# Optimization experiments

Hardware: AMD Instinct MI355X
Metric: run time of the kernel (lower is better)

The kernel has to match this reference:

```python
import jax, jax.numpy as jnp
import numpy as np

B, T, IN = 8, 1000, 80
CONV = 256
CCEP = 222            # ltv_out_channels
FFT_SIZE = 1024
HOP = 256
WIN = 2 * HOP         # 512
PAD = (FFT_SIZE - CCEP) // 2   # 401
NFFT = 2048


def _conv1d_same(x, W, b, groups):
    # x: (B,T,C); W: (O, C//groups, 3); equivalent to torch Conv1d pad=2 then [1:-1]
    y = jax.lax.conv_general_dilated(
        jnp.transpose(x, (0, 2, 1)), W, (1,), [(1, 1)],
        feature_group_count=groups,
        dimension_numbers=('NCH', 'OIH', 'NCH'))
    return jnp.transpose(y, (0, 2, 1)) + b


def _forward(x, z, W1, b1, W2, b2, W3, b3, W4, b4):
    Bx, Tx, _ = x.shape
    # ---- ConvLayers ----
    h = jax.nn.relu(_conv1d_same(x, W1, b1, 1))
    h = jax.nn.relu(_conv1d_same(h, W2, b2, 8))
    h = jax.nn.relu(_conv1d_same(h, W3, b3, 8))
    ccep = _conv1d_same(h, W4, b4, 1)            # (B,T,222)
    q = jnp.arange(1, CCEP // 2 + 1, dtype=x.dtype)
    quef = jnp.concatenate([q[::-1], q])          # [111..1,1..111]
    ccep = ccep / quef
    # ---- ccep -> impulse (log-magnitude cepstrum -> minimum-ish phase impulse) ----
    c = jnp.pad(ccep, ((0, 0), (0, 0), (PAD, PAD)))           # (B,T,1024)
    Y = jnp.fft.fft(c, n=FFT_SIZE, axis=-1)
    mag = jnp.power(10.0, Y.real)
    imp = jnp.fft.ifft(mag * jnp.exp(1j * Y.imag), n=FFT_SIZE, axis=-1).real  # (B,T,1024)
    # ---- time-varying impulse convolution (cross-correlation per frame) ----
    L = z.shape[-1]
    zz = z.reshape(Bx, 1, L)
    zp = jnp.pad(zz, ((0, 0), (0, 0), (WIN // 2 - 1, WIN // 2)))
    starts = jnp.arange(Tx) * HOP
    frames = zp[:, :, starts[:, None] + jnp.arange(WIN)]       # (B,1,T,512)
    fp = jnp.pad(frames, ((0, 0), (0, 0), (0, 0), (FFT_SIZE // 2 - 1, FFT_SIZE // 2)))  # len 1535
    # corr[s] = sum_k fp[s+k] * imp[k], s in [0,512); linear corr via zero-padded FFT
    Fz = jnp.fft.rfft(fp, n=NFFT, axis=-1)                     # (B,1,T,NFFT//2+1)
    Fy = jnp.fft.rfft(imp, n=NFFT, axis=-1)[:, None]           # (B,1,T,NFFT//2+1)
    corr = jnp.fft.irfft(Fz * jnp.conj(Fy), n=NFFT, axis=-1)[..., :WIN]  # (B,1,T,512)
    # ---- overlap-add ----
    n = jnp.arange(WIN, dtype=x.dtype)
    win = 0.5 * (1.0 - jnp.cos(2.0 * jnp.pi * n / WIN))        # periodic hann, win_norm=1
    zw = corr * win
    l, r = zw[..., :HOP], zw[..., HOP:]
    out = l + jnp.roll(r, 1, axis=2)
    return out.reshape(Bx, 1, Tx * HOP)


def setup_inputs() -> dict:
    key = jax.random.key(0)
    ks = jax.random.split(key, 12)
    x = jax.random.normal(ks[0], (B, T, IN), dtype=jnp.float32)
    z = jax.random.normal(ks[1], (B, 1, T * HOP), dtype=jnp.float32)
    def w(k, o, i, kk, scale):
        return jax.random.normal(k, (o, i, kk), dtype=jnp.float32) * (scale / np.sqrt(i * kk))
    W1 = w(ks[2], CONV, IN, 3, 1.0)
    b1 = jnp.zeros((CONV,), jnp.float32)
    W2 = w(ks[3], CONV, CONV // 8, 3, 1.0)
    b2 = jnp.zeros((CONV,), jnp.float32)
    W3 = w(ks[4], CONV, CONV // 8, 3, 1.0)
    b3 = jnp.zeros((CONV,), jnp.float32)
    W4 = w(ks[5], CCEP, CONV, 3, 0.01)   # small scale keeps 10**(.) well-conditioned
    b4 = jnp.zeros((CCEP,), jnp.float32)
    return {"x": x, "z": z, "W1": W1, "b1": b1, "W2": W2, "b2": b2,
            "W3": W3, "b3": b3, "W4": W4, "b4": b4}


def reference(x, z, W1, b1, W2, b2, W3, b3, W4, b4):
    return _forward(x, z, W1, b1, W2, b2, W3, b3, W4, b4)
```

## Files before the change

kernel.cpp:

```cpp
#include <hip/hip_runtime.h>
#include <hip/hip_bf16.h>

#define T_LEN 1000
#define B_N 8
#define IN_CH 80
#define CONV_CH 256
#define CCEP_N 222

typedef short s8v __attribute__((ext_vector_type(8)));
typedef float f16v __attribute__((ext_vector_type(16)));

#define TWO_PI 6.28318530717958647692f

__global__ __launch_bounds__(256) void k_prep(
    const float* __restrict__ W1, const float* __restrict__ W2,
    const float* __restrict__ W3, const float* __restrict__ W4,
    float* __restrict__ Wt1, float* __restrict__ Wt2, float* __restrict__ Wt3,
    __hip_bfloat16* __restrict__ Wc, float2* __restrict__ twTab,
    float* __restrict__ winTab) {
  const int bid = blockIdx.x, tid = threadIdx.x;
  if (bid < 240) {
    int e = bid * 256 + tid;
    int o = e / 240, k = e - o * 240;
    Wt1[k * 256 + o] = W1[e];
  } else if (bid < 336) {
    int e = (bid - 240) * 256 + tid;
    int o = e / 96, k = e - o * 96;
    Wt2[k * 256 + o] = W2[e];
  } else if (bid < 432) {
    int e = (bid - 336) * 256 + tid;
    int o = e / 96, k = e - o * 96;
    Wt3[k * 256 + o] = W3[e];
  } else if (bid < 1200) {
    int e = (bid - 432) * 256 + tid;
    int kloc = e & 31, n = (e >> 5) & 255, chg = e >> 13;
    int kp = chg * 32 + kloc;
    int kappa = kp >> 8, i = kp & 255;
    float v = 0.f;
    if (n < CCEP_N) {
      float invq = 1.f / (float)((n < 111) ? (111 - n) : (n - 110));
      v = W4[n * 768 + i * 3 + kappa] * invq;
    }
    Wc[e] = __float2bfloat16(v);
  } else {
    int e = (bid - 1200) * 256 + tid;
    if (e < 1020) {
      int Q, off;
      if (e < 768)       { Q = 256; off = 0; }
      else if (e < 960)  { Q = 64;  off = 768; }
      else if (e < 1008) { Q = 16;  off = 960; }
      else               { Q = 4;   off = 1008; }
      int rem = e - off;
      int r = rem / Q, pos = rem - r * Q;
      float ang = (TWO_PI * (float)((r + 1) * pos)) / (float)(4 * Q);
      float s, c;
      sincosf(ang, &s, &c);
      twTab[e] = make_float2(c, s);
    } else if (e < 1532) {
      int n = e - 1020;
      winTab[n] = (0.5f - 0.5f * cosf(TWO_PI * (float)n / 512.f)) * (1.f / 1024.f);
    }
  }
}

__global__ __launch_bounds__(256) void k_convall(const float* __restrict__ x,
    const float* __restrict__ Wt1, const float* __restrict__ b1,
    const float* __restrict__ Wt2, const float* __restrict__ b2,
    const float* __restrict__ Wt3, const float* __restrict__ b3,
    __hip_bfloat16* __restrict__ out) {
  const int b = blockIdx.y;
  const int t0 = blockIdx.x * 10;
  const int o = threadIdx.x;
  const int cb = (o >> 5) << 5;
  __shared__ float xs[IN_CH * 18];
  __shared__ float hs1[CONV_CH * 14];
  __shared__ float hs2[CONV_CH * 14];
  for (int e = threadIdx.x; e < 16 * IN_CH; e += 256) {
    int r = e / IN_CH, c = e - r * IN_CH;
    int t = t0 - 3 + r;
    xs[c * 18 + r] = (t >= 0 && t < T_LEN) ? x[(b * T_LEN + t) * IN_CH + c] : 0.f;
  }
  __syncthreads();
  {
    float acc[14];
    float bv = b1[o];
#pragma unroll
    for (int j = 0; j < 14; j++) acc[j] = bv;
    for (int i = 0; i < IN_CH; i++) {
      float w0 = Wt1[(3 * i + 0) * 256 + o];
      float w1 = Wt1[(3 * i + 1) * 256 + o];
      float w2 = Wt1[(3 * i + 2) * 256 + o];
      const float* row = &xs[i * 18];
      float a[16];
#pragma unroll
      for (int u = 0; u < 8; u++) *(float2*)&a[2 * u] = *(const float2*)(row + 2 * u);
#pragma unroll
      for (int j = 0; j < 14; j++) {
        acc[j] = fmaf(a[j], w0, acc[j]);
        acc[j] = fmaf(a[j + 1], w1, acc[j]);
        acc[j] = fmaf(a[j + 2], w2, acc[j]);
      }
    }
#pragma unroll
    for (int j = 0; j < 14; j++) {
      int t = t0 - 2 + j;
      hs1[o * 14 + j] = (t >= 0 && t < T_LEN) ? fmaxf(acc[j], 0.f) : 0.f;
    }
  }
  __syncthreads();
  {
    float acc[12];
    float bv = b2[o];
#pragma unroll
    for (int j = 0; j < 12; j++) acc[j] = bv;
    for (int i = 0; i < 32; i++) {
      float w0 = Wt2[(3 * i + 0) * 256 + o];
      float w1 = Wt2[(3 * i + 1) * 256 + o];
      float w2 = Wt2[(3 * i + 2) * 256 + o];
      const float* row = &hs1[(cb + i) * 14];
      float a[14];
#pragma unroll
      for (int u = 0; u < 7; u++) *(float2*)&a[2 * u] = *(const float2*)(row + 2 * u);
#pragma unroll
      for (int j = 0; j < 12; j++) {
        acc[j] = fmaf(a[j], w0, acc[j]);
        acc[j] = fmaf(a[j + 1], w1, acc[j]);
        acc[j] = fmaf(a[j + 2], w2, acc[j]);
      }
    }
    __syncthreads();
#pragma unroll
    for (int j = 0; j < 12; j++) {
      int t = t0 - 1 + j;
      hs2[o * 14 + j] = (t >= 0 && t < T_LEN) ? fmaxf(acc[j], 0.f) : 0.f;
    }
  }
  __syncthreads();
  {
    float acc[10];
    float bv = b3[o];
#pragma unroll
    for (int j = 0; j < 10; j++) acc[j] = bv;
    for (int i = 0; i < 32; i++) {
      float w0 = Wt3[(3 * i + 0) * 256 + o];
      float w1 = Wt3[(3 * i + 1) * 256 + o];
      float w2 = Wt3[(3 * i + 2) * 256 + o];
      const float* row = &hs2[(cb + i) * 14];
      float a[12];
#pragma unroll
      for (int u = 0; u < 6; u++) *(float2*)&a[2 * u] = *(const float2*)(row + 2 * u);
#pragma unroll
      for (int j = 0; j < 10; j++) {
        acc[j] = fmaf(a[j], w0, acc[j]);
        acc[j] = fmaf(a[j + 1], w1, acc[j]);
        acc[j] = fmaf(a[j + 2], w2, acc[j]);
      }
    }
#pragma unroll
    for (int j = 0; j < 10; j++)
      out[(b * T_LEN + t0 + j) * CONV_CH + o] = __float2bfloat16(fmaxf(acc[j], 0.f));
  }
}

#define APITCH 264
#define BPITCH 40
#define PSTRIDE 1792000
__global__ __launch_bounds__(256) void k_conv4m(
    const __hip_bfloat16* __restrict__ h3, const __hip_bfloat16* __restrict__ Wc,
    const float* __restrict__ bias, float* __restrict__ Pbase) {
  const int mb = blockIdx.x, b = blockIdx.y, ks = blockIdx.z;
  float* __restrict__ P = Pbase + (size_t)ks * PSTRIDE;
  const int t0 = mb * 64;
  const int tid = threadIdx.x;
  const int w = tid >> 6, lane = tid & 63;
  const int wm = w >> 1, wn = w & 1;
  const int lm = lane & 31, half = lane >> 5;

  __shared__ short h3s[67 * APITCH];
  __shared__ short Bs[2][256 * BPITCH];

  const ushort* h3u = (const ushort*)h3;
  for (int g = tid; g < 67 * 64; g += 256) {
    int rr = g >> 6, c4 = g & 63;
    int t = t0 + rr - 1;
    uint2 v = make_uint2(0u, 0u);
    if (t >= 0 && t < T_LEN)
      v = *(const uint2*)(h3u + (b * T_LEN + t) * CONV_CH + c4 * 4);
    *(uint2*)(h3s + rr * APITCH + c4 * 4) = v;
  }

  const ushort* Wu = (const ushort*)(Wc) + (size_t)(ks * 6) * 8192;
#pragma unroll
  for (int it = 0; it < 4; ++it) {
    int idx = (it * 256 + tid) * 8;
    uint4 v = *(const uint4*)(Wu + idx);
    int n = idx >> 5, kloc = idx & 31;
    *(uint4*)(Bs[0] + n * BPITCH + kloc) = v;
  }
  __syncthreads();

  f16v acc0 = {}, acc1 = {}, acc2 = {}, acc3 = {};

  for (int ch = 0; ch < 6; ++ch) {
    const int p = ch & 1;
    if (ch < 5) {
      const ushort* src = Wu + (ch + 1) * 8192;
#pragma unroll
      for (int it = 0; it < 4; ++it) {
        int idx = (it * 256 + tid) * 8;
        uint4 v = *(const uint4*)(src + idx);
        int n = idx >> 5, kloc = idx & 31;
        *(uint4*)(Bs[p ^ 1] + n * BPITCH + kloc) = v;
      }
    }
#pragma unroll
    for (int s = 0; s < 2; ++s) {
      int k0 = ks * 192 + ch * 32 + s * 16;
      int kappa = k0 >> 8, i0 = k0 & 255;
      s8v a = *(const s8v*)(h3s + (wm * 32 + lm + kappa) * APITCH + i0 + half * 8);
      const short* bp = Bs[p] + (wn * 128 + lm) * BPITCH + s * 16 + half * 8;
      s8v b0 = *(const s8v*)(bp);
      s8v b1 = *(const s8v*)(bp + 32 * BPITCH);
      s8v b2 = *(const s8v*)(bp + 64 * BPITCH);
      s8v b3 = *(const s8v*)(bp + 96 * BPITCH);
      acc0 = __builtin_amdgcn_mfma_f32_32x32x16_bf16(a, b0, acc0, 0, 0, 0);
      acc1 = __builtin_amdgcn_mfma_f32_32x32x16_bf16(a, b1, acc1, 0, 0, 0);
      acc2 = __builtin_amdgcn_mfma_f32_32x32x16_bf16(a, b2, acc2, 0, 0, 0);
      acc3 = __builtin_amdgcn_mfma_f32_32x32x16_bf16(a, b3, acc3, 0, 0, 0);
    }
    __syncthreads();
  }

  const int col = lm;
#pragma unroll
  for (int nt = 0; nt < 4; ++nt) {
    int c = wn * 128 + nt * 32 + col;
    if (c >= CCEP_N) continue;
    float bq = 0.f;
    if (ks == 0) {
      float invq = 1.f / (float)((c < 111) ? (111 - c) : (c - 110));
      bq = bias[c] * invq;
    }
    const f16v* A = (nt == 0) ? &acc0 : (nt == 1) ? &acc1 : (nt == 2) ? &acc2 : &acc3;
#pragma unroll
    for (int reg = 0; reg < 16; ++reg) {
      int row = (reg & 3) + 8 * (reg >> 2) + 4 * half;
      int t = t0 + wm * 32 + row;
      if (t < T_LEN)
        P[(size_t)(b * T_LEN + t) * 224 + c] = (*A)[reg] + bq;
    }
  }
}

__device__ __forceinline__ float2 cmul(float2 a, float2 b) {
  return make_float2(fmaf(a.x, b.x, -(a.y * b.y)), fmaf(a.x, b.y, a.y * b.x));
}
__device__ __forceinline__ float2 cadd(float2 a, float2 b) { return make_float2(a.x + b.x, a.y + b.y); }
__device__ __forceinline__ float2 csub(float2 a, float2 b) { return make_float2(a.x - b.x, a.y - b.y); }

#define LIDX(i) ((i) + ((i) >> 2))

template <int Q, int OFF>
__device__ __forceinline__ void fwd_stage2(float2* __restrict__ A,
    float2* __restrict__ B, const float2* __restrict__ Tw, int j) {
  const int pos = j & (Q - 1);
  const int base = ((j - pos) << 2) + pos;
  float2 e1 = Tw[OFF + pos], e2 = Tw[OFF + Q + pos], e3 = Tw[OFF + 2 * Q + pos];
  const float2 w1 = make_float2(e1.x, -e1.y);
  const float2 w2 = make_float2(e2.x, -e2.y);
  const float2 w3 = make_float2(e3.x, -e3.y);
#pragma unroll
  for (int arr = 0; arr < 2; ++arr) {
    float2* X = arr ? B : A;
    float2 a = X[LIDX(base)], b = X[LIDX(base + Q)];
    float2 cc = X[LIDX(base + 2 * Q)], d = X[LIDX(base + 3 * Q)];
    float2 t0 = cadd(a, cc), t1 = csub(a, cc), t2 = cadd(b, d), bd = csub(b, d);
    float2 t3 = make_float2(bd.y, -bd.x);
    X[LIDX(base)]         = cadd(t0, t2);
    X[LIDX(base + Q)]     = cmul(cadd(t1, t3), w1);
    X[LIDX(base + 2 * Q)] = cmul(csub(t0, t2), w2);
    X[LIDX(base + 3 * Q)] = cmul(csub(t1, t3), w3);
  }
}

template <int Q, int OFF>
__device__ __forceinline__ void inv_stage_t(float2* __restrict__ X,
    const float2* __restrict__ Tw, int j) {
  const int pos = j & (Q - 1);
  const int base = ((j - pos) << 2) + pos;
  const float2 w1 = Tw[OFF + pos];
  const float2 w2 = Tw[OFF + Q + pos];
  const float2 w3 = Tw[OFF + 2 * Q + pos];
  float2 a = X[LIDX(base)];
  float2 b = cmul(X[LIDX(base + Q)], w1);
  float2 cc = cmul(X[LIDX(base + 2 * Q)], w2);
  float2 d = cmul(X[LIDX(base + 3 * Q)], w3);
  float2 t0 = cadd(a, cc), t1 = csub(a, cc), t2 = cadd(b, d), bd = csub(b, d);
  float2 t3 = make_float2(-bd.y, bd.x);
  X[LIDX(base)]         = cadd(t0, t2);
  X[LIDX(base + Q)]     = cadd(t1, t3);
  X[LIDX(base + 2 * Q)] = csub(t0, t2);
  X[LIDX(base + 3 * Q)] = csub(t1, t3);
}

__device__ __forceinline__ int rev4d(int v) {
  return ((v & 3) << 6) | (((v >> 2) & 3) << 4) | (((v >> 4) & 3) << 2) | ((v >> 6) & 3);
}

__global__ __launch_bounds__(256) void k_fft(const float* __restrict__ Pb,
    const float* __restrict__ z, const float2* __restrict__ twg,
    const float* __restrict__ wing, float* __restrict__ out,
    float* __restrict__ sbl, float* __restrict__ sbr) {
  const int u = blockIdx.x, b = blockIdx.y;
  const int tA = 2 * u, tB = tA + 1;
  const int btA = b * T_LEN + tA, btB = btA + 1;
  const int j = threadIdx.x;
  __shared__ float2 WlA[1280];
  __shared__ float2 WlB[1280];
  __shared__ float2 Tws[1020];
  for (int e = j; e < 1020; e += 256) Tws[e] = twg[e];

  const float* zb = z + b * 256000;
  float f0A = 0.f, fS, f1B = 0.f;
  {
    int zi0 = tA * 256 + j - 255;
    f0A = (zi0 >= 0) ? zb[zi0] : 0.f;
    fS = zb[tA * 256 + j + 1];
    int zi2 = tB * 256 + j + 1;
    f1B = (zi2 < 256000) ? zb[zi2] : 0.f;
  }
  float c1A = 0.f, c2A = 0.f, c1B = 0.f, c2B = 0.f;
  if (j >= 145) {
    int mA = btA * 224 + (j - 145), mB = btB * 224 + (j - 145);
    c1A = (Pb[mA] + Pb[mA + PSTRIDE]) + (Pb[mA + 2 * PSTRIDE] + Pb[mA + 3 * PSTRIDE]);
    c1B = (Pb[mB] + Pb[mB + PSTRIDE]) + (Pb[mB + 2 * PSTRIDE] + Pb[mB + 3 * PSTRIDE]);
  }
  if (j < 111) {
    int mA = btA * 224 + (j + 111), mB = btB * 224 + (j + 111);
    c2A = (Pb[mA] + Pb[mA + PSTRIDE]) + (Pb[mA + 2 * PSTRIDE] + Pb[mA + 3 * PSTRIDE]);
    c2B = (Pb[mB] + Pb[mB + PSTRIDE]) + (Pb[mB + 2 * PSTRIDE] + Pb[mB + 3 * PSTRIDE]);
  }
  __syncthreads();

  {
    float2 e1 = Tws[j], e2 = Tws[256 + j], e3 = Tws[512 + j];
    const float2 w1 = make_float2(e1.x, -e1.y);
    const float2 w2 = make_float2(e2.x, -e2.y);
    const float2 w3 = make_float2(e3.x, -e3.y);
    {
      float2 t0 = make_float2(c2A, f0A);
      float2 t1 = make_float2(-c2A, f0A);
      float2 t2 = make_float2(c1A, fS);
      float2 t3 = make_float2(fS, -c1A);
      WlA[LIDX(j)]       = cadd(t0, t2);
      WlA[LIDX(j + 256)] = cmul(cadd(t1, t3), w1);
      WlA[LIDX(j + 512)] = cmul(csub(t0, t2), w2);
      WlA[LIDX(j + 768)] = cmul(csub(t1, t3), w3);
    }
    {
      float2 t0 = make_float2(c2B, fS);
      float2 t1 = make_float2(-c2B, fS);
      float2 t2 = make_float2(c1B, f1B);
      float2 t3 = make_float2(f1B, -c1B);
      WlB[LIDX(j)]       = cadd(t0, t2);
      WlB[LIDX(j + 256)] = cmul(cadd(t1, t3), w1);
      WlB[LIDX(j + 512)] = cmul(csub(t0, t2), w2);
      WlB[LIDX(j + 768)] = cmul(csub(t1, t3), w3);
    }
  }
  __syncthreads();

  fwd_stage2<64, 768>(WlA, WlB, Tws, j);  __syncthreads();
  fwd_stage2<16, 960>(WlA, WlB, Tws, j);  __syncthreads();
  fwd_stage2<4, 1008>(WlA, WlB, Tws, j);  __syncthreads();

  const int base = 4 * j;
  float2 XA[4], XB[4];
  {
    float2 u0 = WlA[LIDX(base)], u1 = WlA[LIDX(base + 1)];
    float2 u2 = WlA[LIDX(base + 2)], u3 = WlA[LIDX(base + 3)];
    float2 t0 = cadd(u0, u2), t1 = csub(u0, u2), t2 = cadd(u1, u3), bd = csub(u1, u3);
    float2 t3 = make_float2(bd.y, -bd.x);
    XA[0] = cadd(t0, t2); XA[1] = cadd(t1, t3); XA[2] = csub(t0, t2); XA[3] = csub(t1, t3);
  }
  {
    float2 u0 = WlB[LIDX(base)], u1 = WlB[LIDX(base + 1)];
    float2 u2 = WlB[LIDX(base + 2)], u3 = WlB[LIDX(base + 3)];
    float2 t0 = cadd(u0, u2), t1 = csub(u0, u2), t2 = cadd(u1, u3), bd = csub(u1, u3);
    float2 t3 = make_float2(bd.y, -bd.x);
    XB[0] = cadd(t0, t2); XB[1] = cadd(t1, t3); XB[2] = csub(t0, t2); XB[3] = csub(t1, t3);
  }
#pragma unroll
  for (int q = 0; q < 4; ++q) { WlA[LIDX(base + q)] = XA[q]; WlB[LIDX(base + q)] = XB[q]; }
  __syncthreads();

  const int r0 = rev4d(j);
  const bool self0 = (r0 == 0);
  const int jp = self0 ? 0 : rev4d((256 - r0) & 255);
  float2 PA[4], PB[4];
#pragma unroll
  for (int q = 0; q < 4; ++q) { PA[q] = WlA[LIDX(4 * jp + q)]; PB[q] = WlB[LIDX(4 * jp + q)]; }
  float2 Z[4];
#pragma unroll
  for (int q = 0; q < 4; ++q) {
    float2 SA, SB;
    {
      float2 A = XA[q];
      float2 Bc = self0 ? PA[(4 - q) & 3] : PA[3 - q];
      float2 Y = make_float2(0.5f * (A.x + Bc.x), 0.5f * (A.y - Bc.y));
      float2 F = make_float2(0.5f * (A.y + Bc.y), -0.5f * (A.x - Bc.x));
      float mag = __expf(Y.x * 2.30258509299404568402f);
      float sy, cy;
      __sincosf(Y.y, &sy, &cy);
      float gr = mag * cy, gi = mag * sy;
      SA = make_float2(fmaf(F.x, gr, F.y * gi), fmaf(F.x, gi, -(F.y * gr)));
    }
    {
      float2 A = XB[q];
      float2 Bc = self0 ? PB[(4 - q) & 3] : PB[3 - q];
      float2 Y = make_float2(0.5f * (A.x + Bc.x), 0.5f * (A.y - Bc.y));
      float2 F = make_float2(0.5f * (A.y + Bc.y), -0.5f * (A.x - Bc.x));
      float mag = __expf(Y.x * 2.30258509299404568402f);
      float sy, cy;
      __sincosf(Y.y, &sy, &cy);
      float gr = mag * cy, gi = mag * sy;
      SB = make_float2(fmaf(F.x, gr, F.y * gi), fmaf(F.x, gi, -(F.y * gr)));
    }
    Z[q] = make_float2(SA.x - SB.y, SA.y + SB.x);
  }
  __syncthreads();

  {
    float2 t0 = cadd(Z[0], Z[2]), t1 = csub(Z[0], Z[2]), t2 = cadd(Z[1], Z[3]), bd = csub(Z[1], Z[3]);
    float2 t3 = make_float2(-bd.y, bd.x);
    WlA[LIDX(base)]     = cadd(t0, t2);
    WlA[LIDX(base + 1)] = cadd(t1, t3);
    WlA[LIDX(base + 2)] = csub(t0, t2);
    WlA[LIDX(base + 3)] = csub(t1, t3);
  }
  __syncthreads();

  inv_stage_t<4, 1008>(WlA, Tws, j);  __syncthreads();
  inv_stage_t<16, 960>(WlA, Tws, j);  __syncthreads();
  inv_stage_t<64, 768>(WlA, Tws, j);  __syncthreads();

  {
    float2 w1 = Tws[j], w2 = Tws[256 + j], w3 = Tws[512 + j];
    float2 a = WlA[LIDX(j)];
    float2 bb = cmul(WlA[LIDX(j + 256)], w1);
    float2 cc = cmul(WlA[LIDX(j + 512)], w2);
    float2 d = cmul(WlA[LIDX(j + 768)], w3);
    float2 t0 = cadd(a, cc), t1 = csub(a, cc), t2 = cadd(bb, d), bd = csub(bb, d);
    float2 t3 = make_float2(-bd.y, bd.x);
    float2 Cj    = cadd(t0, t2);
    float2 Cj256 = cadd(t1, t3);
    int n1 = 511 - j, n2 = 255 - j;
    float wn1 = wing[n1], wn2 = wing[n2];
    float vA_l = Cj256.x * wn2;
    float vAB  = Cj.x * wn1 + Cj256.y * wn2;
    float vB_r = Cj.y * wn1;
    out[(b * T_LEN + tB) * 256 + n2] = vAB;
    int su = (b * 500 + u) * 256 + n2;
    sbl[su] = vA_l;
    sbr[su] = vB_r;
  }
}

__global__ __launch_bounds__(256) void k_even(const float* __restrict__ sbl,
    const float* __restrict__ sbr, float* __restrict__ out) {
  int idx = blockIdx.x * 256 + threadIdx.x;
  int n = idx & 255;
  int bu = idx >> 8;
  int u = bu % 500, b = bu / 500;
  int up = (u == 0) ? 499 : u - 1;
  out[(b * T_LEN + 2 * u) * 256 + n] = sbl[idx] + sbr[(b * 500 + up) * 256 + n];
}

extern "C" void kernel_launch(void* const* d_in, const int* in_sizes, int n_in,
                              void* d_out, int out_size, void* d_ws, size_t ws_size,
                              hipStream_t stream) {
  const float* x  = (const float*)d_in[0];
  const float* z  = (const float*)d_in[1];
  const float* W1 = (const float*)d_in[2];
  const float* b1 = (const float*)d_in[3];
  const float* W2 = (const float*)d_in[4];
  const float* b2 = (const float*)d_in[5];
  const float* W3 = (const float*)d_in[6];
  const float* b3 = (const float*)d_in[7];
  const float* W4 = (const float*)d_in[8];
  const float* b4 = (const float*)d_in[9];

  float* ws   = (float*)d_ws;
  __hip_bfloat16* h3bf = (__hip_bfloat16*)ws;
  float* Pb   = ws + 1024000;
  float* sbl  = ws + 8192000;
  float* sbr  = ws + 9216000;
  float* Wt1  = ws + 10240000;
  float* Wt2  = ws + 10301440;
  float* Wt3  = ws + 10326016;
  __hip_bfloat16* Wc = (__hip_bfloat16*)(ws + 10350592);
  float2* twTab = (float2*)(ws + 10448896);
  float* winTab = ws + 10450944;
  float* out = (float*)d_out;

  dim3 blk(256);
  k_prep<<<1206, blk, 0, stream>>>(W1, W2, W3, W4, Wt1, Wt2, Wt3, Wc,
                                   twTab, winTab);

  dim3 cgrid10(T_LEN / 10, B_N);
  k_convall<<<cgrid10, blk, 0, stream>>>(x, Wt1, b1, Wt2, b2, Wt3, b3, h3bf);
  dim3 g4(16, B_N, 4);
  k_conv4m<<<g4, blk, 0, stream>>>(h3bf, Wc, b4, Pb);
  dim3 gf(T_LEN / 2, B_N);
  k_fft<<<gf, blk, 0, stream>>>(Pb, z, twTab, winTab, out, sbl, sbr);
  k_even<<<4000, blk, 0, stream>>>(sbl, sbr, out);
}
```

Before: 176.8 us.

## Split conv stack time rows across two thread halves with vectorized weight loads

```diff
diff --git a/kernel.cpp b/kernel.cpp
--- a/kernel.cpp
+++ b/kernel.cpp
@@ -21,16 +21,22 @@
   const int bid = blockIdx.x, tid = threadIdx.x;
   if (bid < 240) {
     int e = bid * 256 + tid;
-    int o = e / 240, k = e - o * 240;
-    Wt1[k * 256 + o] = W1[e];
+    int i = e % 80;
+    int r = e / 80;
+    int o = r & 255, kap = r >> 8;
+    Wt1[e] = W1[o * 240 + i * 3 + kap];
   } else if (bid < 336) {
     int e = (bid - 240) * 256 + tid;
-    int o = e / 96, k = e - o * 96;
-    Wt2[k * 256 + o] = W2[e];
+    int i = e & 31;
+    int r = e >> 5;
+    int o = r & 255, kap = r >> 8;
+    Wt2[e] = W2[o * 96 + i * 3 + kap];
   } else if (bid < 432) {
     int e = (bid - 336) * 256 + tid;
-    int o = e / 96, k = e - o * 96;
-    Wt3[k * 256 + o] = W3[e];
+    int i = e & 31;
+    int r = e >> 5;
+    int o = r & 255, kap = r >> 8;
+    Wt3[e] = W3[o * 96 + i * 3 + kap];
   } else if (bid < 1200) {
     int e = (bid - 432) * 256 + tid;
     int kloc = e & 31, n = (e >> 5) & 255, chg = e >> 13;
@@ -63,102 +69,108 @@
   }
 }
 
-__global__ __launch_bounds__(256) void k_convall(const float* __restrict__ x,
+template <int SH, int NJ, int NI4, int PITCH, int NA2>
+__device__ __forceinline__ void conv_acc(const float* __restrict__ abase,
+    const float* __restrict__ w0p, const float* __restrict__ w1p,
+    const float* __restrict__ w2p, float* __restrict__ acc) {
+#pragma unroll 2
+  for (int ig = 0; ig < NI4; ++ig) {
+    float4 w0 = *(const float4*)(w0p + 4 * ig);
+    float4 w1 = *(const float4*)(w1p + 4 * ig);
+    float4 w2 = *(const float4*)(w2p + 4 * ig);
+#pragma unroll
+    for (int s = 0; s < 4; ++s) {
+      const float* row = abase + (4 * ig + s) * PITCH;
+      float a[2 * NA2];
+#pragma unroll
+      for (int u = 0; u < NA2; ++u)
+        *(float2*)&a[2 * u] = *(const float2*)(row + 2 * u);
+      const float f0 = ((const float*)&w0)[s];
+      const float f1 = ((const float*)&w1)[s];
+      const float f2 = ((const float*)&w2)[s];
+#pragma unroll
+      for (int jl = 0; jl < NJ; ++jl) {
+        acc[jl] = fmaf(a[jl + SH], f0, acc[jl]);
+        acc[jl] = fmaf(a[jl + SH + 1], f1, acc[jl]);
+        acc[jl] = fmaf(a[jl + SH + 2], f2, acc[jl]);
+      }
+    }
+  }
+}
+
+__global__ __launch_bounds__(512, 6) void k_convall(const float* __restrict__ x,
     const float* __restrict__ Wt1, const float* __restrict__ b1,
     const float* __restrict__ Wt2, const float* __restrict__ b2,
     const float* __restrict__ Wt3, const float* __restrict__ b3,
     __hip_bfloat16* __restrict__ out) {
   const int b = blockIdx.y;
   const int t0 = blockIdx.x * 10;
-  const int o = threadIdx.x;
+  const int tid = threadIdx.x;
+  const int o = tid & 255;
+  const int th = tid >> 8;
   const int cb = (o >> 5) << 5;
   __shared__ float xs[IN_CH * 18];
   __shared__ float hs1[CONV_CH * 14];
   __shared__ float hs2[CONV_CH * 14];
-  for (int e = threadIdx.x; e < 16 * IN_CH; e += 256) {
+  for (int e = tid; e < 16 * IN_CH; e += 512) {
     int r = e / IN_CH, c = e - r * IN_CH;
     int t = t0 - 3 + r;
     xs[c * 18 + r] = (t >= 0 && t < T_LEN) ? x[(b * T_LEN + t) * IN_CH + c] : 0.f;
   }
   __syncthreads();
   {
-    float acc[14];
-    float bv = b1[o];
-#pragma unroll
-    for (int j = 0; j < 14; j++) acc[j] = bv;
-    for (int i = 0; i < IN_CH; i++) {
-      float w0 = Wt1[(3 * i + 0) * 256 + o];
-      float w1 = Wt1[(3 * i + 1) * 256 + o];
-      float w2 = Wt1[(3 * i + 2) * 256 + o];
-      const float* row = &xs[i * 18];
-      float a[16];
-#pragma unroll
-      for (int u = 0; u < 8; u++) *(float2*)&a[2 * u] = *(const float2*)(row + 2 * u);
-#pragma unroll
-      for (int j = 0; j < 14; j++) {
-        acc[j] = fmaf(a[j], w0, acc[j]);
-        acc[j] = fmaf(a[j + 1], w1, acc[j]);
-        acc[j] = fmaf(a[j + 2], w2, acc[j]);
-      }
-    }
-#pragma unroll
-    for (int j = 0; j < 14; j++) {
-      int t = t0 - 2 + j;
-      hs1[o * 14 + j] = (t >= 0 && t < T_LEN) ? fmaxf(acc[j], 0.f) : 0.f;
-    }
-  }
-  __syncthreads();
-  {
-    float acc[12];
-    float bv = b2[o];
-#pragma unroll
-    for (int j = 0; j < 12; j++) acc[j] = bv;
-    for (int i = 0; i < 32; i++) {
-      float w0 = Wt2[(3 * i + 0) * 256 + o];
-      float w1 = Wt2[(3 * i + 1) * 256 + o];
-      float w2 = Wt2[(3 * i + 2) * 256 + o];
-      const float* row = &hs1[(cb + i) * 14];
-      float a[14];
-#pragma unroll
-      for (int u = 0; u < 7; u++) *(float2*)&a[2 * u] = *(const float2*)(row + 2 * u);
-#pragma unroll
-      for (int j = 0; j < 12; j++) {
-        acc[j] = fmaf(a[j], w0, acc[j]);
-        acc[j] = fmaf(a[j + 1], w1, acc[j]);
-        acc[j] = fmaf(a[j + 2], w2, acc[j]);
-      }
-    }
-    __syncthreads();
-#pragma unroll
-    for (int j = 0; j < 12; j++) {
+    float acc[7];
+    const float bv = b1[o];
+#pragma unroll
+    for (int jl = 0; jl < 7; ++jl) acc[jl] = bv;
+    const float* w0p = Wt1 + o * 80;
+    const float* w1p = Wt1 + (256 + o) * 80;
+    const float* w2p = Wt1 + (512 + o) * 80;
+    if (th == 0)
+      conv_acc<0, 7, 20, 18, 5>(&xs[0], w0p, w1p, w2p, acc);
+    else
+      conv_acc<1, 7, 20, 18, 5>(&xs[6], w0p, w1p, w2p, acc);
+#pragma unroll
+    for (int jl = 0; jl < 7; ++jl) {
+      int rr = th * 7 + jl;
+      int t = t0 - 2 + rr;
+      hs1[o * 14 + rr] = (t >= 0 && t < T_LEN) ? fmaxf(acc[jl], 0.f) : 0.f;
+    }
+  }
+  __syncthreads();
+  {
+    float acc[6];
+    const float bv = b2[o];
+#pragma unroll
+    for (int jl = 0; jl < 6; ++jl) acc[jl] = bv;
+    const float* w0p = Wt2 + o * 32;
+    const float* w1p = Wt2 + (256 + o) * 32;
+    const float* w2p = Wt2 + (512 + o) * 32;
+    conv_acc<0, 6, 8, 14, 4>(&hs1[cb * 14 + th * 6], w0p, w1p, w2p, acc);
+#pragma unroll
+    for (int jl = 0; jl < 6; ++jl) {
+      int j = th * 6 + jl;
       int t = t0 - 1 + j;
-      hs2[o * 14 + j] = (t >= 0 && t < T_LEN) ? fmaxf(acc[j], 0.f) : 0.f;
-    }
-  }
-  __syncthreads();
-  {
-    float acc[10];
-    float bv = b3[o];
-#pragma unroll
-    for (int j = 0; j < 10; j++) acc[j] = bv;
-    for (int i = 0; i < 32; i++) {
-      float w0 = Wt3[(3 * i + 0) * 256 + o];
-      float w1 = Wt3[(3 * i + 1) * 256 + o];
-      float w2 = Wt3[(3 * i + 2) * 256 + o];
-      const float* row = &hs2[(cb + i) * 14];
-      float a[12];
-#pragma unroll
-      for (int u = 0; u < 6; u++) *(float2*)&a[2 * u] = *(const float2*)(row + 2 * u);
-#pragma unroll
-      for (int j = 0; j < 10; j++) {
-        acc[j] = fmaf(a[j], w0, acc[j]);
-        acc[j] = fmaf(a[j + 1], w1, acc[j]);
-        acc[j] = fmaf(a[j + 2], w2, acc[j]);
-      }
-    }
-#pragma unroll
-    for (int j = 0; j < 10; j++)
-      out[(b * T_LEN + t0 + j) * CONV_CH + o] = __float2bfloat16(fmaxf(acc[j], 0.f));
+      hs2[o * 14 + j] = (t >= 0 && t < T_LEN) ? fmaxf(acc[jl], 0.f) : 0.f;
+    }
+  }
+  __syncthreads();
+  {
+    float acc[5];
+    const float bv = b3[o];
+#pragma unroll
+    for (int jl = 0; jl < 5; ++jl) acc[jl] = bv;
+    const float* w0p = Wt3 + o * 32;
+    const float* w1p = Wt3 + (256 + o) * 32;
+    const float* w2p = Wt3 + (512 + o) * 32;
+    if (th == 0)
+      conv_acc<0, 5, 8, 14, 4>(&hs2[cb * 14], w0p, w1p, w2p, acc);
+    else
+      conv_acc<1, 5, 8, 14, 4>(&hs2[cb * 14 + 4], w0p, w1p, w2p, acc);
+#pragma unroll
+    for (int jl = 0; jl < 5; ++jl)
+      out[(b * T_LEN + t0 + th * 5 + jl) * CONV_CH + o] =
+          __float2bfloat16(fmaxf(acc[jl], 0.f));
   }
 }
 
@@ -508,7 +520,8 @@
                                    twTab, winTab);
 
   dim3 cgrid10(T_LEN / 10, B_N);
-  k_convall<<<cgrid10, blk, 0, stream>>>(x, Wt1, b1, Wt2, b2, Wt3, b3, h3bf);
+  dim3 cblk(512);
+  k_convall<<<cgrid10, cblk, 0, stream>>>(x, Wt1, b1, Wt2, b2, Wt3, b3, h3bf);
   dim3 g4(16, B_N, 4);
   k_conv4m<<<g4, blk, 0, stream>>>(h3bf, Wc, b4, Pb);
   dim3 gf(T_LEN / 2, B_N);
```

Result: slower. 288.7 us (+63.3%).

## Retile conv stack over 60-step time tiles and 64-channel slices

Applied to the files above, without the earlier changes.

```diff
diff --git a/kernel.cpp b/kernel.cpp
--- a/kernel.cpp
+++ b/kernel.cpp
@@ -21,16 +21,16 @@
   const int bid = blockIdx.x, tid = threadIdx.x;
   if (bid < 240) {
     int e = bid * 256 + tid;
-    int o = e / 240, k = e - o * 240;
-    Wt1[k * 256 + o] = W1[e];
+    int o = e & 255, s = e >> 8;
+    Wt1[e] = W1[o * 240 + s];
   } else if (bid < 336) {
     int e = (bid - 240) * 256 + tid;
-    int o = e / 96, k = e - o * 96;
-    Wt2[k * 256 + o] = W2[e];
+    int o = e & 255, s = e >> 8;
+    Wt2[e] = W2[o * 96 + s];
   } else if (bid < 432) {
     int e = (bid - 336) * 256 + tid;
-    int o = e / 96, k = e - o * 96;
-    Wt3[k * 256 + o] = W3[e];
+    int o = e & 255, s = e >> 8;
+    Wt3[e] = W3[o * 96 + s];
   } else if (bid < 1200) {
     int e = (bid - 432) * 256 + tid;
     int kloc = e & 31, n = (e >> 5) & 255, chg = e >> 13;
@@ -63,102 +63,110 @@
   }
 }
 
+#define TTILE 60
+#define XP 66
+#define HP 66
+
+template <int NI, int PITCH>
+__device__ __forceinline__ void conv8(const float* __restrict__ act,
+    const float* __restrict__ wb, int l, float* __restrict__ acc) {
+  float cw[24], nw[24];
+#pragma unroll
+  for (int q = 0; q < 24; ++q) cw[q] = wb[(q >> 3) * 256 + (q & 7)];
+  for (int i = 0; i < NI; ++i) {
+    const float* wn = wb + min(i + 1, NI - 1) * 768;
+#pragma unroll
+    for (int q = 0; q < 24; ++q) nw[q] = wn[(q >> 3) * 256 + (q & 7)];
+    float a0 = act[i * PITCH + l];
+    float a1 = act[i * PITCH + l + 1];
+    float a2 = act[i * PITCH + l + 2];
+#pragma unroll
+    for (int oc = 0; oc < 8; ++oc)
+      acc[oc] = fmaf(a0, cw[oc], fmaf(a1, cw[8 + oc], fmaf(a2, cw[16 + oc], acc[oc])));
+#pragma unroll
+    for (int q = 0; q < 24; ++q) cw[q] = nw[q];
+  }
+}
+
 __global__ __launch_bounds__(256) void k_convall(const float* __restrict__ x,
     const float* __restrict__ Wt1, const float* __restrict__ b1,
     const float* __restrict__ Wt2, const float* __restrict__ b2,
     const float* __restrict__ Wt3, const float* __restrict__ b3,
     __hip_bfloat16* __restrict__ out) {
-  const int b = blockIdx.y;
-  const int t0 = blockIdx.x * 10;
-  const int o = threadIdx.x;
-  const int cb = (o >> 5) << 5;
-  __shared__ float xs[IN_CH * 18];
-  __shared__ float hs1[CONV_CH * 14];
-  __shared__ float hs2[CONV_CH * 14];
-  for (int e = threadIdx.x; e < 16 * IN_CH; e += 256) {
-    int r = e / IN_CH, c = e - r * IN_CH;
-    int t = t0 - 3 + r;
-    xs[c * 18 + r] = (t >= 0 && t < T_LEN) ? x[(b * T_LEN + t) * IN_CH + c] : 0.f;
-  }
-  __syncthreads();
-  {
-    float acc[14];
-    float bv = b1[o];
-#pragma unroll
-    for (int j = 0; j < 14; j++) acc[j] = bv;
-    for (int i = 0; i < IN_CH; i++) {
-      float w0 = Wt1[(3 * i + 0) * 256 + o];
-      float w1 = Wt1[(3 * i + 1) * 256 + o];
-      float w2 = Wt1[(3 * i + 2) * 256 + o];
-      const float* row = &xs[i * 18];
-      float a[16];
-#pragma unroll
-      for (int u = 0; u < 8; u++) *(float2*)&a[2 * u] = *(const float2*)(row + 2 * u);
-#pragma unroll
-      for (int j = 0; j < 14; j++) {
-        acc[j] = fmaf(a[j], w0, acc[j]);
-        acc[j] = fmaf(a[j + 1], w1, acc[j]);
-        acc[j] = fmaf(a[j + 2], w2, acc[j]);
+  const int t0 = blockIdx.x * TTILE;
+  const int b  = blockIdx.y;
+  const int O0 = blockIdx.z * 64;
+  const int tid = threadIdx.x;
+  const int l = tid & 63;
+  const int w = tid >> 6;
+  const int wrel = w * 16;
+  const int wo = __builtin_amdgcn_readfirstlane(O0 + wrel);
+  const int ri0 = (w >> 1) * 32;
+
+  __shared__ float xs[IN_CH * XP];
+  __shared__ float h1s[64 * HP];
+  __shared__ float h2s[64 * HP];
+
+  for (int e = tid; e < IN_CH * XP; e += 256) {
+    int tt = e / IN_CH, c = e - tt * IN_CH;
+    int t = t0 - 3 + tt;
+    xs[c * XP + tt] = (t >= 0 && t < T_LEN) ? x[(b * T_LEN + t) * IN_CH + c] : 0.f;
+  }
+  __syncthreads();
+
+  {
+    float acc[16];
+#pragma unroll
+    for (int h = 0; h < 2; ++h) {
+#pragma unroll
+      for (int oc = 0; oc < 8; ++oc) acc[8 * h + oc] = b1[wo + 8 * h + oc];
+      conv8<IN_CH, XP>(xs, Wt1 + wo + 8 * h, l, acc + 8 * h);
+    }
+    int t = t0 - 2 + l;
+    bool v = (t >= 0 && t < T_LEN);
+#pragma unroll
+    for (int oc = 0; oc < 16; ++oc)
+      h1s[(wrel + oc) * HP + l] = v ? fmaxf(acc[oc], 0.f) : 0.f;
+  }
+  __syncthreads();
+
+  {
+    float acc[16];
+#pragma unroll
+    for (int h = 0; h < 2; ++h) {
+#pragma unroll
+      for (int oc = 0; oc < 8; ++oc) acc[8 * h + oc] = b2[wo + 8 * h + oc];
+      conv8<32, HP>(h1s + ri0 * HP, Wt2 + wo + 8 * h, l, acc + 8 * h);
+    }
+    int t = t0 - 1 + l;
+    bool v = (t >= 0 && t < T_LEN);
+#pragma unroll
+    for (int oc = 0; oc < 16; ++oc)
+      h2s[(wrel + oc) * HP + l] = v ? fmaxf(acc[oc], 0.f) : 0.f;
+  }
+  __syncthreads();
+
+  {
+    float acc[16];
+#pragma unroll
+    for (int h = 0; h < 2; ++h) {
+#pragma unroll
+      for (int oc = 0; oc < 8; ++oc) acc[8 * h + oc] = b3[wo + 8 * h + oc];
+      conv8<32, HP>(h2s + ri0 * HP, Wt3 + wo + 8 * h, l, acc + 8 * h);
+    }
+    int t = t0 + l;
+    if (l < TTILE && t < T_LEN) {
+      uint pk[8];
+#pragma unroll
+      for (int q = 0; q < 8; ++q) {
+        __hip_bfloat16 lo = __float2bfloat16(fmaxf(acc[2 * q], 0.f));
+        __hip_bfloat16 hi = __float2bfloat16(fmaxf(acc[2 * q + 1], 0.f));
+        pk[q] = (uint)(*(ushort*)&lo) | ((uint)(*(ushort*)&hi) << 16);
       }
-    }
-#pragma unroll
-    for (int j = 0; j < 14; j++) {
-      int t = t0 - 2 + j;
-      hs1[o * 14 + j] = (t >= 0 && t < T_LEN) ? fmaxf(acc[j], 0.f) : 0.f;
-    }
-  }
-  __syncthreads();
-  {
-    float acc[12];
-    float bv = b2[o];
-#pragma unroll
-    for (int j = 0; j < 12; j++) acc[j] = bv;
-    for (int i = 0; i < 32; i++) {
-      float w0 = Wt2[(3 * i + 0) * 256 + o];
-      float w1 = Wt2[(3 * i + 1) * 256 + o];
-      float w2 = Wt2[(3 * i + 2) * 256 + o];
-      const float* row = &hs1[(cb + i) * 14];
-      float a[14];
-#pragma unroll
-      for (int u = 0; u < 7; u++) *(float2*)&a[2 * u] = *(const float2*)(row + 2 * u);
-#pragma unroll
-      for (int j = 0; j < 12; j++) {
-        acc[j] = fmaf(a[j], w0, acc[j]);
-        acc[j] = fmaf(a[j + 1], w1, acc[j]);
-        acc[j] = fmaf(a[j + 2], w2, acc[j]);
-      }
-    }
-    __syncthreads();
-#pragma unroll
-    for (int j = 0; j < 12; j++) {
-      int t = t0 - 1 + j;
-      hs2[o * 14 + j] = (t >= 0 && t < T_LEN) ? fmaxf(acc[j], 0.f) : 0.f;
-    }
-  }
-  __syncthreads();
-  {
-    float acc[10];
-    float bv = b3[o];
-#pragma unroll
-    for (int j = 0; j < 10; j++) acc[j] = bv;
-    for (int i = 0; i < 32; i++) {
-      float w0 = Wt3[(3 * i + 0) * 256 + o];
-      float w1 = Wt3[(3 * i + 1) * 256 + o];
-      float w2 = Wt3[(3 * i + 2) * 256 + o];
-      const float* row = &hs2[(cb + i) * 14];
-      float a[12];
-#pragma unroll
-      for (int u = 0; u < 6; u++) *(float2*)&a[2 * u] = *(const float2*)(row + 2 * u);
-#pragma unroll
-      for (int j = 0; j < 10; j++) {
-        acc[j] = fmaf(a[j], w0, acc[j]);
-        acc[j] = fmaf(a[j + 1], w1, acc[j]);
-        acc[j] = fmaf(a[j + 2], w2, acc[j]);
-      }
-    }
-#pragma unroll
-    for (int j = 0; j < 10; j++)
-      out[(b * T_LEN + t0 + j) * CONV_CH + o] = __float2bfloat16(fmaxf(acc[j], 0.f));
+      uint4* dst = (uint4*)(out + (size_t)(b * T_LEN + t) * CONV_CH + wo);
+      dst[0] = make_uint4(pk[0], pk[1], pk[2], pk[3]);
+      dst[1] = make_uint4(pk[4], pk[5], pk[6], pk[7]);
+    }
   }
 }
 
@@ -507,8 +515,8 @@
   k_prep<<<1206, blk, 0, stream>>>(W1, W2, W3, W4, Wt1, Wt2, Wt3, Wc,
                                    twTab, winTab);
 
-  dim3 cgrid10(T_LEN / 10, B_N);
-  k_convall<<<cgrid10, blk, 0, stream>>>(x, Wt1, b1, Wt2, b2, Wt3, b3, h3bf);
+  dim3 cgrid(17, B_N, 4);
+  k_convall<<<cgrid, blk, 0, stream>>>(x, Wt1, b1, Wt2, b2, Wt3, b3, h3bf);
   dim3 g4(16, B_N, 4);
   k_conv4m<<<g4, blk, 0, stream>>>(h3bf, Wc, b4, Pb);
   dim3 gf(T_LEN / 2, B_N);
```

Result: slower. 207.9 us (+17.6%).
